# Performance work log

Hardware: AMD Instinct MI355X
Metric: run time of the kernel (lower is better)

## Reference

```python
import jax, jax.numpy as jnp
import numpy as np

MARGIN = 1.0
THETA = 0.1
PI_PAIRS = 4096


def _huber(y):
    # DVIS huber: quadratic below theta, linear (with bias) above
    less_grad_factor = 1.0 / (2.0 * THETA)
    less_loss_bias = less_grad_factor * THETA ** 2
    return jnp.where(y < THETA, y * y * less_grad_factor, y - THETA + less_loss_bias)


def setup_inputs() -> dict:
    key = jax.random.key(0)
    k1, k2 = jax.random.split(key)
    bs, ch, ht, wd = 4, 1, 512, 512
    y_pred = jax.random.normal(k1, (bs, ch, ht, wd), dtype=jnp.float32)
    # instance labels 0..7; 0 = background
    y_true = jax.random.randint(k2, (bs, ch, ht, wd), 0, 8).astype(jnp.int32)
    # replicate no_grad sampling_over_objects: randperm over nonzero (foreground) pixels
    flat = np.asarray(y_true.reshape(bs, ht * wd))
    rng = np.random.default_rng(0)
    smpl = np.stack([rng.permutation(np.nonzero(flat[b])[0])[:PI_PAIRS] for b in range(bs)])
    return {"y_pred": y_pred, "y_true": y_true, "smpl_idxs": jnp.asarray(smpl, jnp.int32)}


def reference(y_pred, y_true, smpl_idxs):
    bs, ch, ht, wd = y_pred.shape  # ch == 1
    pred = jnp.take_along_axis(y_pred.reshape(bs, ht * wd), smpl_idxs, axis=1)  # [bs, P]
    true = jnp.take_along_axis(y_true.reshape(bs, ht * wd), smpl_idxs, axis=1)  # [bs, P] int
    P = pred.shape[1]
    # torch.combinations(x, r=2) -> pairs (x[i], x[j]) with i < j
    a = pred[:, :, None]                     # [bs, P, 1]  first element of pair
    b = jax.nn.relu(pred)[:, None, :]        # [bs, 1, P]  relu of second element
    pi_pred = jnp.abs(jax.nn.relu(a - b))    # [bs, P, P]
    t = (true[:, :, None] == true[:, None, :]).astype(pred.dtype)  # [bs, P, P]
    loss = 3.0 * t * _huber(pi_pred) + (1.0 - t) * _huber(MARGIN - pi_pred)
    mask = jnp.triu(jnp.ones((P, P), dtype=bool), k=1)  # i < j pairs only
    n_pairs = P * (P - 1) // 2
    per_el = jnp.sum(jnp.where(mask, loss, 0.0), axis=(1, 2)) / n_pairs
    return jnp.mean(per_el)
```

## Files before the change

kernel.cpp:

```cpp
#include <hip/hip_runtime.h>

#define PP   4096
#define HW   262144
#define BSZ  4
#define NT   32
#define NTRI (NT * (NT + 1) / 2)
#define INV_SCALE (1.0 / (8386560.0 * 4.0))

__global__ __launch_bounds__(256)
void fused_k(const float* __restrict__ y_pred,
             const int*   __restrict__ y_true,
             const int*   __restrict__ smpl,
             float* __restrict__ out) {
    const int b = blockIdx.y;
    const int u = blockIdx.x;
    int tj = (int)((sqrtf(8.0f * (float)u + 1.0f) - 1.0f) * 0.5f);
    while ((tj + 1) * (tj + 2) / 2 <= u) ++tj;
    while (tj * (tj + 1) / 2 > u) --tj;
    const int ti = u - tj * (tj + 1) / 2;

    const int t    = threadIdx.x;
    const int base = b * PP;
    const int boff = b * HW;

    __shared__ float2 si[128];
    __shared__ float2 sj[128];
    if (t < 128) {
        int idx = smpl[base + ti * 128 + t];
        float p = y_pred[boff + idx];
        si[t] = make_float2(p, __int_as_float(y_true[boff + idx]));
    } else {
        int t2  = t - 128;
        int idx = smpl[base + tj * 128 + t2];
        float p = y_pred[boff + idx];
        sj[t2] = make_float2(fmaxf(p, 0.0f), __int_as_float(y_true[boff + idx]));
    }
    __syncthreads();

    const int ig = t & 31;
    const int jg = (t >> 5) * 16;

    float av[4]; int tv[4];
    #pragma unroll
    for (int m = 0; m < 4; ++m) {
        float2 v = si[ig + 32 * m];
        av[m] = v.x;
        tv[m] = __float_as_int(v.y);
    }

    float acc = 0.0f;
    if (ti == tj) {
        #pragma unroll 4
        for (int jj = 0; jj < 16; ++jj) {
            float2 v   = sj[jg + jj];
            int    j   = jg + jj;
            int    tjv = __float_as_int(v.y);
            #pragma unroll
            for (int m = 0; m < 4; ++m) {
                float s  = fmaxf(av[m] - v.x, 0.0f);
                bool  tt = (tv[m] == tjv);
                float y  = tt ? s : (1.0f - s);
                float sc = tt ? 3.0f : 1.0f;
                float mn = fminf(y, 0.1f);
                float h  = fmaf(5.0f * mn, mn, y - mn);
                float l  = sc * h;
                acc += (j > ig + 32 * m) ? l : 0.0f;
            }
        }
    } else {
        #pragma unroll 4
        for (int jj = 0; jj < 16; ++jj) {
            float2 v   = sj[jg + jj];
            int    tjv = __float_as_int(v.y);
            #pragma unroll
            for (int m = 0; m < 4; ++m) {
                float s  = fmaxf(av[m] - v.x, 0.0f);
                bool  tt = (tv[m] == tjv);
                float y  = tt ? s : (1.0f - s);
                float sc = tt ? 3.0f : 1.0f;
                float mn = fminf(y, 0.1f);
                float h  = fmaf(5.0f * mn, mn, y - mn);
                acc = fmaf(sc, h, acc);
            }
        }
    }

    for (int off = 32; off > 0; off >>= 1)
        acc += __shfl_down(acc, off, 64);
    __shared__ float wsum[4];
    const int lane = t & 63, wid = t >> 6;
    if (lane == 0) wsum[wid] = acc;
    __syncthreads();
    if (t == 0) {
        float s = (wsum[0] + wsum[1]) + (wsum[2] + wsum[3]);
        atomicAdd(out, s * (float)INV_SCALE);
    }
}

extern "C" void kernel_launch(void* const* d_in, const int* in_sizes, int n_in,
                              void* d_out, int out_size, void* d_ws, size_t ws_size,
                              hipStream_t stream) {
    const float* y_pred = (const float*)d_in[0];
    const int*   y_true = (const int*)d_in[1];
    const int*   smpl   = (const int*)d_in[2];
    float* out = (float*)d_out;

    fused_k<<<dim3(NTRI, BSZ), dim3(256), 0, stream>>>(y_pred, y_true, smpl, out);
}
```

Measured before the change: 91.38 us.

## Compute off-diagonal pair loss in packed fp16 with arithmetic label-match mask

Stores sampled predictions and labels as fp16 in shared memory and evaluates the off-diagonal tile pairs with packed half2 vector math, two rows per instruction. The label-equality branch is replaced by an arithmetic mask (max(1-|ti-tj|,0)) that blends the two huber arguments, and the 3x same-label weight is applied as all + 2*matched. The goal is to halve ALU instruction count in the dominant loop. It costs precision: predictions are rounded to fp16 and per-thread partial sums accumulate in fp16, which may drift from the fp32 reference.

```diff
diff --git a/kernel.cpp b/kernel.cpp
--- a/kernel.cpp
+++ b/kernel.cpp
@@ -6,6 +6,17 @@
 #define NT   32
 #define NTRI (NT * (NT + 1) / 2)
 #define INV_SCALE (1.0 / (8386560.0 * 4.0))
+
+
+typedef _Float16 h2 __attribute__((ext_vector_type(2)));
+union HU { unsigned u; h2 v; };
+union HS { unsigned short u; _Float16 h; };
+
+__device__ __forceinline__ h2 u_h2(unsigned x) { HU c; c.u = x; return c.v; }
+__device__ __forceinline__ unsigned h2_u(h2 x) { HU c; c.v = x; return c.u; }
+__device__ __forceinline__ h2 h2splat(float f) {
+    h2 r; r.x = (_Float16)f; r.y = (_Float16)f; return r;
+}
 
 __global__ __launch_bounds__(256)
 void fused_k(const float* __restrict__ y_pred,
@@ -23,41 +34,96 @@
     const int base = b * PP;
     const int boff = b * HW;
 
-    __shared__ float2 si[128];
-    __shared__ float2 sj[128];
+    __shared__ unsigned si[128];
+    __shared__ uint2    sj[128];
     if (t < 128) {
         int idx = smpl[base + ti * 128 + t];
-        float p = y_pred[boff + idx];
-        si[t] = make_float2(p, __int_as_float(y_true[boff + idx]));
+        float a = y_pred[boff + idx];
+        int   l = y_true[boff + idx];
+        HS ph; ph.h = (_Float16)a;
+        HS lh; lh.h = (_Float16)(float)l;
+        si[t] = (unsigned)ph.u | ((unsigned)lh.u << 16);
     } else {
         int t2  = t - 128;
         int idx = smpl[base + tj * 128 + t2];
-        float p = y_pred[boff + idx];
-        sj[t2] = make_float2(fmaxf(p, 0.0f), __int_as_float(y_true[boff + idx]));
+        float a = y_pred[boff + idx];
+        int   l = y_true[boff + idx];
+        HS pb; pb.h = (_Float16)fmaxf(a, 0.0f);
+        HS lh; lh.h = (_Float16)(float)l;
+        sj[t2] = make_uint2((unsigned)pb.u * 0x10001u,
+                            (unsigned)lh.u * 0x10001u);
     }
     __syncthreads();
 
     const int ig = t & 31;
     const int jg = (t >> 5) * 16;
 
-    float av[4]; int tv[4];
-    #pragma unroll
-    for (int m = 0; m < 4; ++m) {
-        float2 v = si[ig + 32 * m];
-        av[m] = v.x;
-        tv[m] = __float_as_int(v.y);
-    }
+    float acc = 0.0f;
 
-    float acc = 0.0f;
-    if (ti == tj) {
+    if (ti != tj) {
+        const unsigned w0 = si[ig], w1 = si[ig + 32], w2 = si[ig + 64], w3 = si[ig + 96];
+        const h2 A01 = u_h2((w0 & 0xFFFFu) | (w1 << 16));
+        const h2 A23 = u_h2((w2 & 0xFFFFu) | (w3 << 16));
+        const h2 T01 = u_h2((w0 >> 16) | (w1 & 0xFFFF0000u));
+        const h2 T23 = u_h2((w2 >> 16) | (w3 & 0xFFFF0000u));
+
+        const h2 one2  = h2splat(1.0f);
+        const h2 zero2 = h2splat(0.0f);
+        const h2 two2  = h2splat(2.0f);
+        const h2 th2   = h2splat(0.1f);
+        const h2 five2 = h2splat(5.0f);
+
+        h2 aA0 = zero2, aM0 = zero2;
+        h2 aA1 = zero2, aM1 = zero2;
+
+        #pragma unroll
+        for (int jj = 0; jj < 16; ++jj) {
+            const uint2 vj = sj[jg + jj];
+            const h2 b2  = u_h2(vj.x);
+            const h2 tl2 = u_h2(vj.y);
+            {
+                h2 ae = __builtin_elementwise_abs(T01 - tl2);
+                h2 mm = __builtin_elementwise_max(one2 - ae, zero2);
+                h2 s  = __builtin_elementwise_max(A01 - b2, zero2);
+                h2 y  = (s * two2 - one2) * mm + (one2 - s);
+                h2 mn = __builtin_elementwise_min(y, th2);
+                h2 hh = mn * five2 * mn + (y - mn);
+                aA0 = aA0 + hh;
+                aM0 = aM0 + hh * mm;
+            }
+            {
+                h2 ae = __builtin_elementwise_abs(T23 - tl2);
+                h2 mm = __builtin_elementwise_max(one2 - ae, zero2);
+                h2 s  = __builtin_elementwise_max(A23 - b2, zero2);
+                h2 y  = (s * two2 - one2) * mm + (one2 - s);
+                h2 mn = __builtin_elementwise_min(y, th2);
+                h2 hh = mn * five2 * mn + (y - mn);
+                aA1 = aA1 + hh;
+                aM1 = aM1 + hh * mm;
+            }
+        }
+        float sAll = ((float)aA0.x + (float)aA0.y) + ((float)aA1.x + (float)aA1.y);
+        float sMat = ((float)aM0.x + (float)aM0.y) + ((float)aM1.x + (float)aM1.y);
+        acc = fmaf(2.0f, sMat, sAll);
+    } else {
+        float av[4]; unsigned short tv[4];
+        #pragma unroll
+        for (int m = 0; m < 4; ++m) {
+            unsigned w = si[ig + 32 * m];
+            HS c; c.u = (unsigned short)(w & 0xFFFFu);
+            av[m] = (float)c.h;
+            tv[m] = (unsigned short)(w >> 16);
+        }
         #pragma unroll 4
         for (int jj = 0; jj < 16; ++jj) {
-            float2 v   = sj[jg + jj];
-            int    j   = jg + jj;
-            int    tjv = __float_as_int(v.y);
+            uint2 vj = sj[jg + jj];
+            HS c; c.u = (unsigned short)(vj.x & 0xFFFFu);
+            float bx = (float)c.h;
+            unsigned short tjv = (unsigned short)(vj.y & 0xFFFFu);
+            int j = jg + jj;
             #pragma unroll
             for (int m = 0; m < 4; ++m) {
-                float s  = fmaxf(av[m] - v.x, 0.0f);
+                float s  = fmaxf(av[m] - bx, 0.0f);
                 bool  tt = (tv[m] == tjv);
                 float y  = tt ? s : (1.0f - s);
                 float sc = tt ? 3.0f : 1.0f;
@@ -65,22 +131,6 @@
                 float h  = fmaf(5.0f * mn, mn, y - mn);
                 float l  = sc * h;
                 acc += (j > ig + 32 * m) ? l : 0.0f;
-            }
-        }
-    } else {
-        #pragma unroll 4
-        for (int jj = 0; jj < 16; ++jj) {
-            float2 v   = sj[jg + jj];
-            int    tjv = __float_as_int(v.y);
-            #pragma unroll
-            for (int m = 0; m < 4; ++m) {
-                float s  = fmaxf(av[m] - v.x, 0.0f);
-                bool  tt = (tv[m] == tjv);
-                float y  = tt ? s : (1.0f - s);
-                float sc = tt ? 3.0f : 1.0f;
-                float mn = fminf(y, 0.1f);
-                float h  = fmaf(5.0f * mn, mn, y - mn);
-                acc = fmaf(sc, h, acc);
             }
         }
     }
```

Result: no change. 90.49 us (-1.0%).
